# Optimization experiments

Measured on AMD Instinct MI355X. Metric: run time of the kernel, lower is better.

Reference implementation:

```python
import jax, jax.numpy as jnp
import numpy as np

EPS = 1e-5  # torch LayerNorm default

def _ln(x, g, b):
    m = x.mean(-1, keepdims=True)
    v = x.var(-1, keepdims=True)  # biased var, matches torch LayerNorm
    return (x - m) * jax.lax.rsqrt(v + EPS) * g + b

def setup_inputs() -> dict:
    key = jax.random.key(0)
    ks = jax.random.split(key, 8)
    B, T, D, H, depth, C = 64, 512, 1024, 1024, 2, 1024
    return {
        'input': jax.random.normal(ks[0], (B, T, D), jnp.float32),
        'w_ih': jax.random.normal(ks[1], (depth, 4 * H, D), jnp.float32),
        'b_ih': jax.random.normal(ks[2], (depth, 4 * H), jnp.float32),
        'w_hh': jax.random.normal(ks[3], (depth, 4 * H, H), jnp.float32),
        'b_hh': jax.random.normal(ks[4], (depth, 4 * H), jnp.float32),
        'g_ih': jax.random.uniform(ks[5], (depth, 4 * H), jnp.float32),
        'be_ih': jnp.zeros((depth, 4 * H), jnp.float32),
        'g_hh': jax.random.uniform(ks[6], (depth, 4 * H), jnp.float32),
        'be_hh': jnp.zeros((depth, 4 * H), jnp.float32),
        'g_ho': jax.random.uniform(ks[7], (depth, H), jnp.float32),
        'be_ho': jnp.zeros((depth, H), jnp.float32),
        'fc_w': jax.random.normal(jax.random.fold_in(key, 9), (C, H), jnp.float32),
        'fc_b': jnp.zeros((C,), jnp.float32),
    }

def reference(input, w_ih, b_ih, w_hh, b_hh, g_ih, be_ih, g_hh, be_hh, g_ho, be_ho, fc_w, fc_b):
    B, T, D = input.shape
    depth, four_h, H = w_hh.shape
    H = four_h // 4
    h0 = jnp.zeros((depth, B, H), input.dtype)
    c0 = jnp.zeros((depth, B, H), input.dtype)
    xs = jnp.swapaxes(input, 0, 1)  # [T, B, D]

    def step(carry, x_t):
        h, c = carry
        x = x_t
        new_h, new_c = [], []
        for l in range(depth):  # small fixed layer loop
            gates = (_ln(x @ w_ih[l].T + b_ih[l], g_ih[l], be_ih[l])
                     + _ln(h[l] @ w_hh[l].T + b_hh[l], g_hh[l], be_hh[l]))  # [B, 4H]
            i, f, o = jnp.split(jax.nn.sigmoid(gates[:, :3 * H]), 3, axis=1)
            g = jnp.tanh(gates[:, 3 * H:])
            cy = f * c[l] + i * g
            hy = o * jnp.tanh(_ln(cy, g_ho[l], be_ho[l]))
            new_h.append(hy)
            new_c.append(cy)
            x = hy
        return (jnp.stack(new_h), jnp.stack(new_c)), x

    _, ys = jax.lax.scan(step, (h0, c0), xs)  # ys: [T, B, H] (top-layer h)
    out = jnp.swapaxes(ys, 0, 1).reshape(B * T, H) @ fc_w.T + fc_b
    return out.reshape(B, T, -1)
```

## Files before the change

kernel.cpp:

```cpp
#include <hip/hip_runtime.h>


typedef __attribute__((ext_vector_type(8))) short short8;
typedef __attribute__((ext_vector_type(8))) __bf16 bf16x8;
typedef __attribute__((ext_vector_type(4))) float f32x4;
typedef __attribute__((ext_vector_type(4))) unsigned short us4;
typedef unsigned long long u64;

#define B_ 64
#define T_ 512
#define D_ 1024
#define H_ 1024
#define FH_ 4096
#define LAG_ 16
#define NSPAN 16
#define SPANS 33
#define RCH_ (B_ * 16)

#define SMEM_WHH 131072
#define SMEM_STRIP 8448
#define SMEM_TOTAL (SMEM_WHH + SMEM_STRIP + 1024)

typedef const __attribute__((address_space(1))) unsigned int* gas_ptr;
typedef __attribute__((address_space(3))) unsigned int* las_ptr;
#define GLOAD_LDS16(g, l) \
  __builtin_amdgcn_global_load_lds((gas_ptr)(g), (las_ptr)(l), 16, 0, 0)

#define ALD(p)    __hip_atomic_load((p), __ATOMIC_RELAXED, __HIP_MEMORY_SCOPE_AGENT)
#define ALD64(p)  __hip_atomic_load((p), __ATOMIC_RELAXED, __HIP_MEMORY_SCOPE_AGENT)
#define AST(p, v) __hip_atomic_store((p), (v), __ATOMIC_RELAXED, __HIP_MEMORY_SCOPE_AGENT)

static __device__ __forceinline__ unsigned short f2bf(float f) {
  unsigned int u = __builtin_bit_cast(unsigned int, f);
  u += 0x7FFFu + ((u >> 16) & 1u);
  return (unsigned short)(u >> 16);
}
static __device__ __forceinline__ float bf2f(unsigned short u) {
  unsigned int x = ((unsigned int)u) << 16;
  return __builtin_bit_cast(float, x);
}

__global__ void cast_split_k(const float4* __restrict__ in,
                             us4* __restrict__ hi, us4* __restrict__ lo, int n4) {
  int i = blockIdx.x * 256 + threadIdx.x;
  if (i < n4) {
    float4 v = in[i];
    us4 h, l;
    h[0] = f2bf(v.x); l[0] = f2bf(v.x - bf2f(h[0]));
    h[1] = f2bf(v.y); l[1] = f2bf(v.y - bf2f(h[1]));
    h[2] = f2bf(v.z); l[2] = f2bf(v.z - bf2f(h[2]));
    h[3] = f2bf(v.w); l[3] = f2bf(v.w - bf2f(h[3]));
    hi[i] = h; lo[i] = l;
  }
}

__global__ void transpose_split_k(const float4* __restrict__ x,
                                  us4* __restrict__ hi, us4* __restrict__ lo) {
  int i = blockIdx.x * 256 + threadIdx.x;
  int d4  = i & 255;
  int rem = i >> 8;
  int b = rem & 63;
  int t = rem >> 6;
  float4 v = x[((size_t)(b * T_ + t) << 8) + d4];
  us4 h, l;
  h[0] = f2bf(v.x); l[0] = f2bf(v.x - bf2f(h[0]));
  h[1] = f2bf(v.y); l[1] = f2bf(v.y - bf2f(h[1]));
  h[2] = f2bf(v.z); l[2] = f2bf(v.z - bf2f(h[2]));
  h[3] = f2bf(v.w); l[3] = f2bf(v.w - bf2f(h[3]));
  size_t o = ((size_t)(t * B_ + b) << 8) + d4;
  hi[o] = h; lo[o] = l;
}

__global__ void whh_frag3_k(const float* __restrict__ w_hh,
                            unsigned short* __restrict__ frag) {
  int i = blockIdx.x * 256 + threadIdx.x;
  int lane = i & 63;
  int kc   = (i >> 6) & 31;
  int g    = (i >> 11) & 1;
  int sel  = (i >> 12) & 1;
  int j    = (i >> 13) & 127;
  int layer= (i >> 20) & 1;
  int fc = lane & 15;
  int gc = (g * 2 + (fc >> 3)) * 1024 + j * 8 + (fc & 7);
  int k0 = kc * 32 + (lane >> 4) * 8;
  const float* src = w_hh + ((size_t)layer * FH_ + gc) * 1024 + k0;
  short8 o;
#pragma unroll
  for (int e = 0; e < 8; ++e) {
    float v = src[e];
    unsigned short h = f2bf(v);
    o[e] = sel ? (short)f2bf(v - bf2f(h)) : (short)h;
  }
  *(short8*)(frag + (size_t)i * 8) = o;
}

template <int FCMODE>
__global__ __launch_bounds__(256) void gemm3_k(
    const unsigned short* __restrict__ Ahi, const unsigned short* __restrict__ Alo,
    const unsigned short* __restrict__ Whi, const unsigned short* __restrict__ Wlo,
    const float* __restrict__ bias, float* __restrict__ out, int K, int N) {
  __shared__ unsigned short lAh[128 * 40];
  __shared__ unsigned short lAl[128 * 40];
  __shared__ unsigned short lWh[128 * 40];
  __shared__ unsigned short lWl[128 * 40];
  int tid = threadIdx.x;
  int l = tid & 63, w = tid >> 6;
  int r0 = blockIdx.y * 128, c0 = blockIdx.x * 128;
  int wr = (w >> 1) * 64, wc = (w & 1) * 64;
  int lr = l & 15, lk = (l >> 4) * 8;
  f32x4 acc[4][4] = {};
  int srow = tid >> 2;
  int scc  = (tid & 3) * 8;

  for (int kt = 0; kt < K; kt += 32) {
#pragma unroll
    for (int i = 0; i < 2; ++i) {
      int row = srow + i * 64;
      size_t aoff = (size_t)(r0 + row) * K + kt + scc;
      size_t woff = (size_t)(c0 + row) * K + kt + scc;
      *(short8*)&lAh[row * 40 + scc] = *(const short8*)(Ahi + aoff);
      *(short8*)&lAl[row * 40 + scc] = *(const short8*)(Alo + aoff);
      *(short8*)&lWh[row * 40 + scc] = *(const short8*)(Whi + woff);
      *(short8*)&lWl[row * 40 + scc] = *(const short8*)(Wlo + woff);
    }
    __syncthreads();
    bf16x8 ah[4], al[4], bh[4], bl[4];
#pragma unroll
    for (int mi = 0; mi < 4; ++mi) {
      ah[mi] = *(bf16x8*)&lAh[(wr + mi * 16 + lr) * 40 + lk];
      al[mi] = *(bf16x8*)&lAl[(wr + mi * 16 + lr) * 40 + lk];
    }
#pragma unroll
    for (int ni = 0; ni < 4; ++ni) {
      bh[ni] = *(bf16x8*)&lWh[(wc + ni * 16 + lr) * 40 + lk];
      bl[ni] = *(bf16x8*)&lWl[(wc + ni * 16 + lr) * 40 + lk];
    }
#pragma unroll
    for (int mi = 0; mi < 4; ++mi)
#pragma unroll
      for (int ni = 0; ni < 4; ++ni) {
        acc[mi][ni] = __builtin_amdgcn_mfma_f32_16x16x32_bf16(ah[mi], bh[ni], acc[mi][ni], 0, 0, 0);
        acc[mi][ni] = __builtin_amdgcn_mfma_f32_16x16x32_bf16(ah[mi], bl[ni], acc[mi][ni], 0, 0, 0);
        acc[mi][ni] = __builtin_amdgcn_mfma_f32_16x16x32_bf16(al[mi], bh[ni], acc[mi][ni], 0, 0, 0);
      }
    __syncthreads();
  }

#pragma unroll
  for (int mi = 0; mi < 4; ++mi)
#pragma unroll
    for (int ni = 0; ni < 4; ++ni)
#pragma unroll
      for (int reg = 0; reg < 4; ++reg) {
        int r = r0 + wr + mi * 16 + (l >> 4) * 4 + reg;
        int c = c0 + wc + ni * 16 + lr;
        float v = acc[mi][ni][reg] + bias[c];
        if (FCMODE) {
          int b = r & 63, t = r >> 6;
          out[((size_t)b * T_ + t) * (size_t)N + c] = v;
        } else {
          out[(size_t)r * N + c] = v;
        }
      }
}

struct SpanP {
  const unsigned short* whhF;
  const float *P0, *P1;
  unsigned short *hpHi, *hpLo;
  unsigned short *XYhi, *XYlo;
  float* cst;
  const float *bhh, *gih, *beih, *ghh, *behh, *gho, *beho;
  float *part1, *part2;
  float *stats1, *stats2;
  unsigned *cnt;
  int s0;
};

#define CSET(set, layer) (p.cnt + ((set) * 2 + (layer)) * 128)

static __device__ __forceinline__ void waitc(const unsigned* c, unsigned tgt) {
  if (threadIdx.x < 64) {
    int l = threadIdx.x;
    for (;;) {
      unsigned v = 0xffffffffu;
      if (l < 8) v = ALD(c + l * 16);
#pragma unroll
      for (int o = 4; o; o >>= 1) {
        unsigned u = (unsigned)__shfl_xor((int)v, o);
        v = v < u ? v : u;
      }
      v = (unsigned)__shfl((int)v, 0);
      if (v >= tgt) break;
      __builtin_amdgcn_s_sleep(2);
    }
  }
  __syncthreads();
}

__global__ __launch_bounds__(512) void span_k(SpanP p) {
  extern __shared__ char smem[];
  unsigned short* wl = (unsigned short*)smem;
  float* ldshh = (float*)(smem + SMEM_WHH);
  float* statsL = (float*)(smem + SMEM_WHH + SMEM_STRIP);
  __shared__ float red8[8];

  const int tid = threadIdx.x;
  const int blk = blockIdx.x;
  const int layer = blk >> 7;
  const int j = blk & 127;
  const int w = tid >> 6, l = tid & 63;
  const int lr = l & 15, lq = l >> 4;
  const int slayer = blk >> 6;
  const int srow = blk & 63;
  const int row = tid >> 3, c8 = tid & 7;
  const int hcol = j * 8 + c8;
  const int subj = j & 7;
  const int subs = srow & 7;

  {
    const unsigned short* gsrc = p.whhF + ((size_t)blk << 16);
#pragma unroll
    for (int r = 0; r < 16; ++r) {
      int c = r * 512 + tid;
      GLOAD_LDS16(gsrc + (size_t)c * 8, wl + (size_t)c * 8);
    }
  }

  float gihv[4], beihv[4], ghhv[4], behhv[4];
#pragma unroll
  for (int q = 0; q < 4; ++q) {
    int gc = layer * FH_ + q * 1024 + hcol;
    gihv[q] = p.gih[gc]; beihv[q] = p.beih[gc];
    ghhv[q] = p.ghh[gc]; behhv[q] = p.behh[gc];
  }
  float ghov  = p.gho[layer * H_ + hcol];
  float behov = p.beho[layer * H_ + hcol];
  const int gch = w & 1;
  const int q4 = gch * 2 + (lr >> 3);
  const float bhhv = p.bhh[layer * FH_ + q4 * 1024 + j * 8 + (lr & 7)];
  float creg = p.cst[((size_t)(layer * B_ + row)) * H_ + hcol];

  __syncthreads();

  for (int sl = 0; sl < NSPAN; ++sl) {
    const int s = p.s0 + sl;
    const unsigned g = (unsigned)(s + 1);
    const int t0 = layer ? (s - LAG_) : s;
    const bool active = (t0 >= 0) && (t0 < T_);
    const int slotp = (sl - 1) & 15;
    const int slot = sl;

    waitc(CSET(4, layer), 16u * (g - 1));
    float ih[4] = {0, 0, 0, 0}, hh[4] = {0, 0, 0, 0};
    if (active) {
      const float* Pb = layer ? p.P1 : p.P0;
#pragma unroll
      for (int q = 0; q < 4; ++q)
        ih[q] = Pb[((size_t)(sl * B_ + row)) * FH_ + q * 1024 + hcol];

      const int rf = w >> 1;
      const int rowbase = rf * 16;
      const unsigned short* hHb = p.hpHi + ((size_t)(slotp * 2 + layer)) * 65536;
      const unsigned short* hLb = p.hpLo + ((size_t)(slotp * 2 + layer)) * 65536;
      f32x4 acc = {};
#pragma unroll 8
      for (int kc = 0; kc < 32; ++kc) {
        int k = kc * 32 + lq * 8;
        bf16x8 ah = __builtin_bit_cast(bf16x8, *(const short8*)(hHb + (rowbase + lr) * 1024 + k));
        bf16x8 al = __builtin_bit_cast(bf16x8, *(const short8*)(hLb + (rowbase + lr) * 1024 + k));
        bf16x8 bh = __builtin_bit_cast(bf16x8, *(const short8*)&wl[(size_t)(gch * 2048 + kc * 64 + l) * 8]);
        bf16x8 bl = __builtin_bit_cast(bf16x8, *(const short8*)&wl[(size_t)(4096 + gch * 2048 + kc * 64 + l) * 8]);
        acc = __builtin_amdgcn_mfma_f32_16x16x32_bf16(ah, bh, acc, 0, 0, 0);
        acc = __builtin_amdgcn_mfma_f32_16x16x32_bf16(al, bh, acc, 0, 0, 0);
        acc = __builtin_amdgcn_mfma_f32_16x16x32_bf16(ah, bl, acc, 0, 0, 0);
      }
      int bc = q4 * 8 + (lr & 7);
#pragma unroll
      for (int reg = 0; reg < 4; ++reg)
        ldshh[(rowbase + lq * 4 + reg) * 33 + bc] = acc[reg] + bhhv;
    }
    __syncthreads();
    if (active) {
      float s1 = 0, q1 = 0, s2 = 0, q2 = 0;
#pragma unroll
      for (int q = 0; q < 4; ++q) {
        float a = ih[q];
        float b = ldshh[row * 33 + q * 8 + c8];
        hh[q] = b;
        s1 += a; q1 += a * a; s2 += b; q2 += b * b;
      }
#pragma unroll
      for (int o = 1; o < 8; o <<= 1) {
        s1 += __shfl_xor(s1, o); q1 += __shfl_xor(q1, o);
        s2 += __shfl_xor(s2, o); q2 += __shfl_xor(q2, o);
      }
      if (c8 == 0) {
        float* pb = p.part1 + ((size_t)(layer * 64 + row) * 4) * 128 + j;
        AST(pb + 0 * 128, s1); AST(pb + 1 * 128, q1);
        AST(pb + 2 * 128, s2); AST(pb + 3 * 128, q2);
      }
    }
    __syncthreads();
    if (tid == 0) atomicAdd(CSET(0, layer) + subj * 16, 1u);

    if (blk < 128) {
      waitc(CSET(0, slayer), 16u * g);
      int st = tid >> 7, jj = tid & 127;
      float v = ALD(p.part1 + ((size_t)(slayer * 64 + srow) * 4 + st) * 128 + jj);
#pragma unroll
      for (int o = 32; o; o >>= 1) v += __shfl_xor(v, o);
      if (l == 0) red8[w] = v;
      __syncthreads();
      if (tid < 4)
        AST(p.stats1 + (size_t)(slayer * 64 + srow) * 4 + tid, red8[tid * 2] + red8[tid * 2 + 1]);
      __syncthreads();
      if (tid == 0) atomicAdd(CSET(1, slayer) + subs * 16, 1u);
    }

    waitc(CSET(1, layer), 8u * g);
    if (tid < 64) {
      const u64* sp = (const u64*)(p.stats1 + (size_t)layer * 256);
      u64 a = ALD64(sp + tid);
      u64 b = ALD64(sp + 64 + tid);
      ((u64*)statsL)[tid] = a;
      ((u64*)statsL)[64 + tid] = b;
    }
    __syncthreads();
    float ogate = 0.0f;
    if (active) {
      float S1 = statsL[row * 4 + 0], Q1 = statsL[row * 4 + 1];
      float S2 = statsL[row * 4 + 2], Q2 = statsL[row * 4 + 3];
      const float inv4h = 1.0f / 4096.0f;
      float m1 = S1 * inv4h, m2 = S2 * inv4h;
      float i1 = rsqrtf(Q1 * inv4h - m1 * m1 + 1e-5f);
      float i2 = rsqrtf(Q2 * inv4h - m2 * m2 + 1e-5f);
      float pre[4];
#pragma unroll
      for (int q = 0; q < 4; ++q)
        pre[q] = gihv[q] * (ih[q] - m1) * i1 + beihv[q]
               + ghhv[q] * (hh[q] - m2) * i2 + behhv[q];
      float iG = 1.0f / (1.0f + __expf(-pre[0]));
      float fG = 1.0f / (1.0f + __expf(-pre[1]));
      float oG = 1.0f / (1.0f + __expf(-pre[2]));
      float gG = tanhf(pre[3]);
      creg = fG * creg + iG * gG;
      ogate = oG;
      float sc = creg, sq = creg * creg;
#pragma unroll
      for (int o = 1; o < 8; o <<= 1) { sc += __shfl_xor(sc, o); sq += __shfl_xor(sq, o); }
      if (c8 == 0) {
        float* pb = p.part2 + ((size_t)(layer * 64 + row) * 2) * 128 + j;
        AST(pb + 0 * 128, sc); AST(pb + 1 * 128, sq);
      }
    }
    __syncthreads();
    if (tid == 0) atomicAdd(CSET(2, layer) + subj * 16, 1u);

    if (blk < 128) {
      waitc(CSET(2, slayer), 16u * g);
      if (tid < 256) {
        int st = tid >> 7, jj = tid & 127;
        float v = ALD(p.part2 + ((size_t)(slayer * 64 + srow) * 2 + st) * 128 + jj);
#pragma unroll
        for (int o = 32; o; o >>= 1) v += __shfl_xor(v, o);
        if (l == 0) red8[w] = v;
      }
      __syncthreads();
      if (tid < 2)
        AST(p.stats2 + (size_t)(slayer * 64 + srow) * 2 + tid, red8[tid * 2] + red8[tid * 2 + 1]);
      __syncthreads();
      if (tid == 0) atomicAdd(CSET(3, slayer) + subs * 16, 1u);
    }

    waitc(CSET(3, layer), 8u * g);
    if (tid < 64) {
      const u64* sp2 = (const u64*)(p.stats2 + (size_t)layer * 128);
      ((u64*)statsL)[tid] = ALD64(sp2 + tid);
    }
    __syncthreads();
    if (active) {
      float S3 = statsL[row * 2 + 0], Q3 = statsL[row * 2 + 1];
      const float invh = 1.0f / 1024.0f;
      float m3 = S3 * invh;
      float i3 = rsqrtf(Q3 * invh - m3 * m3 + 1e-5f);
      float hy = ogate * tanhf((creg - m3) * i3 * ghov + behov);
      unsigned hv = f2bf(hy);
      unsigned lv = f2bf(hy - bf2f(hv));
      unsigned hv2 = (unsigned)__shfl_down((int)hv, 1);
      unsigned lv2 = (unsigned)__shfl_down((int)lv, 1);
      if ((c8 & 1) == 0) {
        size_t i32 = (((size_t)(slot * 2 + layer) * 64 + row) * 1024 + hcol) >> 1;
        AST((unsigned*)p.hpHi + i32, hv | (hv2 << 16));
        AST((unsigned*)p.hpLo + i32, lv | (lv2 << 16));
      }
      size_t yo = ((size_t)t0 * B_ + row) * H_ + hcol;
      p.XYhi[yo] = (unsigned short)hv;
      p.XYlo[yo] = (unsigned short)lv;
    }
    __syncthreads();
    if (tid == 0) atomicAdd(CSET(4, layer) + subj * 16, 1u);
  }

  p.cst[((size_t)(layer * B_ + row)) * H_ + hcol] = creg;
}

extern "C" void kernel_launch(void* const* d_in, const int* in_sizes, int n_in,
                              void* d_out, int out_size, void* d_ws, size_t ws_size,
                              hipStream_t stream) {
  const float* x    = (const float*)d_in[0];
  const float* w_ih = (const float*)d_in[1];
  const float* b_ih = (const float*)d_in[2];
  const float* w_hh = (const float*)d_in[3];
  const float* b_hh = (const float*)d_in[4];
  const float* g_ih = (const float*)d_in[5];
  const float* be_ih= (const float*)d_in[6];
  const float* g_hh = (const float*)d_in[7];
  const float* be_hh= (const float*)d_in[8];
  const float* g_ho = (const float*)d_in[9];
  const float* be_ho= (const float*)d_in[10];
  const float* fc_w = (const float*)d_in[11];
  const float* fc_b = (const float*)d_in[12];
  float* out = (float*)d_out;
  (void)ws_size; (void)in_sizes; (void)n_in; (void)out_size;

  char* wsb = (char*)d_ws;
  size_t off = 0;
  unsigned short* wihHi  = (unsigned short*)(wsb + off); off += 16777216;
  unsigned short* wihLo  = (unsigned short*)(wsb + off); off += 16777216;
  unsigned short* whhF   = (unsigned short*)(wsb + off); off += 33554432;
  unsigned short* fcHi   = (unsigned short*)(wsb + off); off += 2097152;
  unsigned short* fcLo   = (unsigned short*)(wsb + off); off += 2097152;
  unsigned short* XYhi   = (unsigned short*)(wsb + off); off += 67108864;
  unsigned short* XYlo   = (unsigned short*)(wsb + off); off += 67108864;
  float* P0              = (float*)(wsb + off); off += (size_t)16 * B_ * FH_ * 4;
  float* P1              = (float*)(wsb + off); off += (size_t)16 * B_ * FH_ * 4;
  unsigned short* hpHi   = (unsigned short*)(wsb + off); off += 4194304;
  unsigned short* hpLo   = (unsigned short*)(wsb + off); off += 4194304;
  float* cst             = (float*)(wsb + off); off += 524288;
  float* part1           = (float*)(wsb + off); off += 524288;
  float* part2           = (float*)(wsb + off); off += 262144;
  float* stats1          = (float*)(wsb + off); off += 2048;
  float* stats2          = (float*)(wsb + off); off += 1024;
  unsigned* cnt          = (unsigned*)(wsb + off); off += 5120;

  {
    int n4 = 2 * FH_ * D_ / 4;
    cast_split_k<<<(n4 + 255) / 256, 256, 0, stream>>>((const float4*)w_ih, (us4*)wihHi, (us4*)wihLo, n4);
    int nf = H_ * H_ / 4;
    cast_split_k<<<(nf + 255) / 256, 256, 0, stream>>>((const float4*)fc_w, (us4*)fcHi, (us4*)fcLo, nf);
    int nx = T_ * B_ * D_ / 4;
    transpose_split_k<<<nx / 256, 256, 0, stream>>>((const float4*)x, (us4*)XYhi, (us4*)XYlo);
    whh_frag3_k<<<8192, 256, 0, stream>>>(w_hh, whhF);
  }

  hipMemsetAsync(hpHi, 0, 8388608, stream);
  hipMemsetAsync(cst, 0, 524288, stream);
  hipMemsetAsync(cnt, 0, 5120, stream);

  hipFuncSetAttribute(reinterpret_cast<const void*>(span_k),
                      hipFuncAttributeMaxDynamicSharedMemorySize, SMEM_TOTAL);

  SpanP prm;
  prm.whhF = whhF; prm.P0 = P0; prm.P1 = P1;
  prm.hpHi = hpHi; prm.hpLo = hpLo; prm.XYhi = XYhi; prm.XYlo = XYlo;
  prm.cst = cst;
  prm.bhh = b_hh; prm.gih = g_ih; prm.beih = be_ih;
  prm.ghh = g_hh; prm.behh = be_hh; prm.gho = g_ho; prm.beho = be_ho;
  prm.part1 = part1; prm.part2 = part2; prm.stats1 = stats1; prm.stats2 = stats2;
  prm.cnt = cnt;

  for (int c = 0; c < SPANS; ++c) {
    int s = c * NSPAN;
    if (s < T_) {
      gemm3_k<0><<<dim3(FH_ / 128, RCH_ / 128), 256, 0, stream>>>(
          XYhi + (size_t)s * B_ * D_, XYlo + (size_t)s * B_ * D_,
          wihHi, wihLo, b_ih, P0, D_, FH_);
    }
    if (s >= LAG_) {
      gemm3_k<0><<<dim3(FH_ / 128, RCH_ / 128), 256, 0, stream>>>(
          XYhi + (size_t)(s - LAG_) * B_ * D_, XYlo + (size_t)(s - LAG_) * B_ * D_,
          wihHi + (1 << 22), wihLo + (1 << 22), b_ih + FH_, P1, D_, FH_);
    }
    prm.s0 = s;
    span_k<<<256, 512, SMEM_TOTAL, stream>>>(prm);
  }

  gemm3_k<1><<<dim3(H_ / 128, (T_ * B_) / 128), 256, 0, stream>>>(
      XYhi, XYlo, fcHi, fcLo, fc_b, out, H_, H_);
}
```

Baseline: 19.47 ms.

## Replace two-stage LayerNorm stats reduction with redundant per-block reduction

```diff
diff --git a/kernel.cpp b/kernel.cpp
--- a/kernel.cpp
+++ b/kernel.cpp
@@ -172,7 +172,6 @@
   float* cst;
   const float *bhh, *gih, *beih, *ghh, *behh, *gho, *beho;
   float *part1, *part2;
-  float *stats1, *stats2;
   unsigned *cnt;
   int s0;
 };
@@ -192,7 +191,7 @@
       }
       v = (unsigned)__shfl((int)v, 0);
       if (v >= tgt) break;
-      __builtin_amdgcn_s_sleep(2);
+      __builtin_amdgcn_s_sleep(1);
     }
   }
   __syncthreads();
@@ -203,7 +202,6 @@
   unsigned short* wl = (unsigned short*)smem;
   float* ldshh = (float*)(smem + SMEM_WHH);
   float* statsL = (float*)(smem + SMEM_WHH + SMEM_STRIP);
-  __shared__ float red8[8];
 
   const int tid = threadIdx.x;
   const int blk = blockIdx.x;
@@ -211,12 +209,9 @@
   const int j = blk & 127;
   const int w = tid >> 6, l = tid & 63;
   const int lr = l & 15, lq = l >> 4;
-  const int slayer = blk >> 6;
-  const int srow = blk & 63;
   const int row = tid >> 3, c8 = tid & 7;
   const int hcol = j * 8 + c8;
   const int subj = j & 7;
-  const int subs = srow & 7;
 
   {
     const unsigned short* gsrc = p.whhF + ((size_t)blk << 16);
@@ -251,7 +246,7 @@
     const int slotp = (sl - 1) & 15;
     const int slot = sl;
 
-    waitc(CSET(4, layer), 16u * (g - 1));
+    waitc(CSET(2, layer), 16u * (g - 1));
     float ih[4] = {0, 0, 0, 0}, hh[4] = {0, 0, 0, 0};
     if (active) {
       const float* Pb = layer ? p.P1 : p.P0;
@@ -304,27 +299,20 @@
     __syncthreads();
     if (tid == 0) atomicAdd(CSET(0, layer) + subj * 16, 1u);
 
-    if (blk < 128) {
-      waitc(CSET(0, slayer), 16u * g);
-      int st = tid >> 7, jj = tid & 127;
-      float v = ALD(p.part1 + ((size_t)(slayer * 64 + srow) * 4 + st) * 128 + jj);
-#pragma unroll
-      for (int o = 32; o; o >>= 1) v += __shfl_xor(v, o);
-      if (l == 0) red8[w] = v;
-      __syncthreads();
-      if (tid < 4)
-        AST(p.stats1 + (size_t)(slayer * 64 + srow) * 4 + tid, red8[tid * 2] + red8[tid * 2 + 1]);
-      __syncthreads();
-      if (tid == 0) atomicAdd(CSET(1, slayer) + subs * 16, 1u);
-    }
-
-    waitc(CSET(1, layer), 8u * g);
-    if (tid < 64) {
-      const u64* sp = (const u64*)(p.stats1 + (size_t)layer * 256);
-      u64 a = ALD64(sp + tid);
-      u64 b = ALD64(sp + 64 + tid);
-      ((u64*)statsL)[tid] = a;
-      ((u64*)statsL)[64 + tid] = b;
+    waitc(CSET(0, layer), 16u * g);
+    if (active) {
+      int pp = tid >> 1;
+      const u64* src = (const u64*)(p.part1 +
+          (((size_t)layer * 64 + (pp >> 2)) * 4 + (pp & 3)) * 128) + (tid & 1) * 32;
+      float ssum = 0.0f;
+#pragma unroll
+      for (int i = 0; i < 32; ++i) {
+        u64 v = ALD64(src + i);
+        ssum += __builtin_bit_cast(float, (unsigned)v)
+              + __builtin_bit_cast(float, (unsigned)(v >> 32));
+      }
+      ssum += __shfl_xor(ssum, 1);
+      if ((tid & 1) == 0) statsL[pp] = ssum;
     }
     __syncthreads();
     float ogate = 0.0f;
@@ -355,28 +343,23 @@
       }
     }
     __syncthreads();
-    if (tid == 0) atomicAdd(CSET(2, layer) + subj * 16, 1u);
-
-    if (blk < 128) {
-      waitc(CSET(2, slayer), 16u * g);
-      if (tid < 256) {
-        int st = tid >> 7, jj = tid & 127;
-        float v = ALD(p.part2 + ((size_t)(slayer * 64 + srow) * 2 + st) * 128 + jj);
-#pragma unroll
-        for (int o = 32; o; o >>= 1) v += __shfl_xor(v, o);
-        if (l == 0) red8[w] = v;
-      }
-      __syncthreads();
-      if (tid < 2)
-        AST(p.stats2 + (size_t)(slayer * 64 + srow) * 2 + tid, red8[tid * 2] + red8[tid * 2 + 1]);
-      __syncthreads();
-      if (tid == 0) atomicAdd(CSET(3, slayer) + subs * 16, 1u);
-    }
-
-    waitc(CSET(3, layer), 8u * g);
-    if (tid < 64) {
-      const u64* sp2 = (const u64*)(p.stats2 + (size_t)layer * 128);
-      ((u64*)statsL)[tid] = ALD64(sp2 + tid);
+    if (tid == 0) atomicAdd(CSET(1, layer) + subj * 16, 1u);
+
+    waitc(CSET(1, layer), 16u * g);
+    if (active) {
+      int pp = tid >> 2;
+      const u64* src = (const u64*)(p.part2 +
+          (((size_t)layer * 64 + (pp >> 1)) * 2 + (pp & 1)) * 128) + (tid & 3) * 16;
+      float ssum = 0.0f;
+#pragma unroll
+      for (int i = 0; i < 16; ++i) {
+        u64 v = ALD64(src + i);
+        ssum += __builtin_bit_cast(float, (unsigned)v)
+              + __builtin_bit_cast(float, (unsigned)(v >> 32));
+      }
+      ssum += __shfl_xor(ssum, 1);
+      ssum += __shfl_xor(ssum, 2);
+      if ((tid & 3) == 0) statsL[pp] = ssum;
     }
     __syncthreads();
     if (active) {
@@ -399,7 +382,7 @@
       p.XYlo[yo] = (unsigned short)lv;
     }
     __syncthreads();
-    if (tid == 0) atomicAdd(CSET(4, layer) + subj * 16, 1u);
+    if (tid == 0) atomicAdd(CSET(2, layer) + subj * 16, 1u);
   }
 
   p.cst[((size_t)(layer * B_ + row)) * H_ + hcol] = creg;
@@ -440,9 +423,7 @@
   float* cst             = (float*)(wsb + off); off += 524288;
   float* part1           = (float*)(wsb + off); off += 524288;
   float* part2           = (float*)(wsb + off); off += 262144;
-  float* stats1          = (float*)(wsb + off); off += 2048;
-  float* stats2          = (float*)(wsb + off); off += 1024;
-  unsigned* cnt          = (unsigned*)(wsb + off); off += 5120;
+  unsigned* cnt          = (unsigned*)(wsb + off); off += 3072;
 
   {
     int n4 = 2 * FH_ * D_ / 4;
@@ -456,7 +437,7 @@
 
   hipMemsetAsync(hpHi, 0, 8388608, stream);
   hipMemsetAsync(cst, 0, 524288, stream);
-  hipMemsetAsync(cnt, 0, 5120, stream);
+  hipMemsetAsync(cnt, 0, 3072, stream);
 
   hipFuncSetAttribute(reinterpret_cast<const void*>(span_k),
                       hipFuncAttributeMaxDynamicSharedMemorySize, SMEM_TOTAL);
@@ -467,7 +448,7 @@
   prm.cst = cst;
   prm.bhh = b_hh; prm.gih = g_ih; prm.beih = be_ih;
   prm.ghh = g_hh; prm.behh = be_hh; prm.gho = g_ho; prm.beho = be_ho;
-  prm.part1 = part1; prm.part2 = part2; prm.stats1 = stats1; prm.stats2 = stats2;
+  prm.part1 = part1; prm.part2 = part2;
   prm.cnt = cnt;
 
   for (int c = 0; c < SPANS; ++c) {
```

Result: slower. 27.50 ms (+41.2%).
